# Kernel optimization log

Measured on AMD Instinct MI355X. Metric: run time of the kernel, lower is better.

Reference implementation:

```python
import jax, jax.numpy as jnp
import numpy as np

N_AGENTS = 8192
OBS_DIM = 520
EMBED = 64
HID = 128
N_ACT = 6


def setup_inputs() -> dict:
    key = jax.random.key(0)
    ks = jax.random.split(key, 16)
    s = 0.05  # small init scale for numerical stability
    return {
        "obs": jax.random.normal(ks[0], (N_AGENTS, OBS_DIM), jnp.float32),
        "beliefs": jax.random.normal(ks[1], (N_AGENTS, HID), jnp.float32),
        "W1": jax.random.normal(ks[2], (OBS_DIM, EMBED), jnp.float32) * s,
        "b1": jnp.zeros((EMBED,), jnp.float32),
        "W2": jax.random.normal(ks[3], (EMBED, EMBED), jnp.float32) * s,
        "b2": jnp.zeros((EMBED,), jnp.float32),
        "Wb": jax.random.normal(ks[4], (HID, EMBED), jnp.float32) * s,
        "bb": jnp.zeros((EMBED,), jnp.float32),
        "Wg": jax.random.normal(ks[5], (2 * EMBED, HID), jnp.float32) * s,
        "bg": jnp.zeros((HID,), jnp.float32),
        "Wir": jax.random.normal(ks[6], (HID, HID), jnp.float32) * s,
        "Wiz": jax.random.normal(ks[7], (HID, HID), jnp.float32) * s,
        "Win": jax.random.normal(ks[8], (HID, HID), jnp.float32) * s,
        "Whr": jax.random.normal(ks[9], (HID, HID), jnp.float32) * s,
        "bhr": jnp.zeros((HID,), jnp.float32),
        "Whz": jax.random.normal(ks[10], (HID, HID), jnp.float32) * s,
        "bhz": jnp.zeros((HID,), jnp.float32),
        "Whn": jax.random.normal(ks[11], (HID, HID), jnp.float32) * s,
        "bhn": jnp.zeros((HID,), jnp.float32),
        "Wout": jax.random.normal(ks[12], (HID, N_ACT), jnp.float32) * s,
        "bout": jnp.zeros((N_ACT,), jnp.float32),
    }


def reference(obs, beliefs, W1, b1, W2, b2, Wb, bb, Wg, bg,
              Wir, Wiz, Win, Whr, bhr, Whz, bhz, Whn, bhn, Wout, bout):
    n_agents = obs.shape[0]
    # obs MLP: Dense -> relu -> Dense -> relu  [A, EMBED]
    h_obs = jax.nn.relu(obs @ W1 + b1)
    h_obs = jax.nn.relu(h_obs @ W2 + b2)
    # belief projection [A, EMBED]
    bp = beliefs @ Wb + bb
    # self-attention over beliefs with diagonal masked out
    attn_logits = (bp @ bp.T) / jnp.sqrt(jnp.asarray(EMBED, bp.dtype))
    attn_logits = attn_logits + jnp.eye(n_agents, dtype=bp.dtype) * (-1e8)
    attn_weights = jax.nn.softmax(attn_logits, axis=-1)
    contexts = attn_weights @ bp  # [A, EMBED]
    # GRU input projection [A, HID]
    gru_in = jnp.concatenate([h_obs, contexts], axis=-1) @ Wg + bg
    # flax GRUCell (input denses bias-free, hidden denses biased)
    r = jax.nn.sigmoid(gru_in @ Wir + beliefs @ Whr + bhr)
    z = jax.nn.sigmoid(gru_in @ Wiz + beliefs @ Whz + bhz)
    n = jnp.tanh(gru_in @ Win + r * (beliefs @ Whn + bhn))
    new_beliefs = (1.0 - z) * n + z * beliefs
    logits = new_beliefs @ Wout + bout
    return (logits, new_beliefs)
```

## Files before the change

### kernel.cpp

```cpp
#include <hip/hip_runtime.h>

#define A_N 8192
#define OBS_D 520
#define EMB 64
#define HID 128
#define NACT 6
#define SPLIT 16

typedef short bf16x8 __attribute__((ext_vector_type(8)));
typedef _Float16 half8 __attribute__((ext_vector_type(8)));
typedef float f32x4 __attribute__((ext_vector_type(4)));
typedef unsigned short u16;
typedef unsigned int u32;

#define MFMA_BF(a,b,c) __builtin_amdgcn_mfma_f32_16x16x32_bf16(a,b,c,0,0,0)
#define MFMA_FH(a,b,c) __builtin_amdgcn_mfma_f32_16x16x32_f16(a,b,c,0,0,0)

__device__ inline u32 fbits(float f){ union{float f; u32 u;}v; v.f=f; return v.u; }
__device__ inline float fval(u32 u){ union{u32 u; float f;}v; v.u=u; return v.f; }
__device__ inline u16 f2bf(float f){ u32 u=fbits(f); u += 0x7fffu + ((u>>16)&1u); return (u16)(u>>16); }
__device__ inline u32 pk_bf(float pe, float po){
  return __builtin_amdgcn_perm(fbits(po), fbits(pe), 0x07060302u);
}
__device__ inline float sigmoidf_fast(float x){
  x = fminf(fmaxf(x, -30.f), 30.f);
  return 1.f / (1.f + __expf(-x));
}
__device__ inline float tanhf_fast(float x){
  x = fminf(fmaxf(x, -15.f), 15.f);
  float e = __expf(-2.f*x);
  return (1.f - e) / (1.f + e);
}

#define EXP2C 0.18033688011112042f

__global__ __launch_bounds__(256) void kPrep2(
    const float* __restrict__ Wg, const float* __restrict__ Wir,
    const float* __restrict__ Wiz, const float* __restrict__ Win,
    const float* __restrict__ Whr, const float* __restrict__ Whz,
    const float* __restrict__ Whn, const float* __restrict__ W1,
    const float* __restrict__ W2, const float* __restrict__ Wb,
    const float* __restrict__ beliefs, const float* __restrict__ bb,
    _Float16* __restrict__ WT, _Float16* __restrict__ W1T,
    _Float16* __restrict__ W2T, u16* __restrict__ bp, u16* __restrict__ bpT)
{
  __shared__ float tile[64][65];
  __shared__ u16 WbL[64][136];
  const int t = threadIdx.x, b = blockIdx.x;

  if (b < 38) {
    const float* src; int k0, c0, srcStride, kValid;
    if (b < 28) {
      const int mi = b >> 2, tl = b & 3;
      src = mi==0?Wg: mi==1?Wir: mi==2?Wiz: mi==3?Win: mi==4?Whr: mi==5?Whz: Whn;
      k0 = (tl >> 1) * 64; c0 = (tl & 1) * 64; srcStride = 128; kValid = 128;
    } else if (b < 37) {
      src = W1; k0 = (b - 28) * 64; c0 = 0; srcStride = 64; kValid = OBS_D;
    } else {
      src = W2; k0 = 0; c0 = 0; srcStride = 64; kValid = 64;
    }
    #pragma unroll
    for (int i = 0; i < 16; i++) {
      const int idx = i * 256 + t;
      const int rr = idx >> 6, cc = idx & 63;
      tile[rr][cc] = (k0 + rr < kValid) ? src[(size_t)(k0 + rr) * srcStride + c0 + cc] : 0.f;
    }
    __syncthreads();
    if (b < 28) {
      const int mi = b >> 2;
      _Float16* dst = WT + (size_t)mi * 16384;
      #pragma unroll
      for (int i = 0; i < 16; i++) {
        const int idx = i * 256 + t;
        const int rr = idx >> 6, cc = idx & 63;
        dst[(size_t)(c0 + rr) * 128 + k0 + cc] = (_Float16)tile[cc][rr];
      }
    } else if (b < 37) {
      #pragma unroll
      for (int i = 0; i < 16; i++) {
        const int idx = i * 256 + t;
        const int rr = idx >> 6, cc = idx & 63;
        if (k0 + cc < 544)
          W1T[(size_t)rr * 544 + k0 + cc] = (_Float16)tile[cc][rr];
      }
    } else {
      #pragma unroll
      for (int i = 0; i < 16; i++) {
        const int idx = i * 256 + t;
        const int rr = idx >> 6, cc = idx & 63;
        W2T[(size_t)rr * 64 + cc] = (_Float16)tile[cc][rr];
      }
    }
  } else {
    const int lane = t & 63, wid = t >> 6;
    const int m = lane & 15, quad = lane >> 4;
    const int r0 = (b - 38) * 64 + wid * 16;

    #pragma unroll
    for (int i = 0; i < 8; i++) {
      const int i4 = i * 256 + t;
      float4 w4 = ((const float4*)Wb)[i4];
      const int k = i4 >> 4, c = (i4 & 15) * 4;
      WbL[c+0][k] = f2bf(w4.x); WbL[c+1][k] = f2bf(w4.y);
      WbL[c+2][k] = f2bf(w4.z); WbL[c+3][k] = f2bf(w4.w);
    }
    __syncthreads();

    f32x4 acc[4];
    #pragma unroll
    for (int ct = 0; ct < 4; ct++) acc[ct] = (f32x4){0.f,0.f,0.f,0.f};
    #pragma unroll
    for (int s = 0; s < 4; s++) {
      const int k0 = s*32;
      const float* ap = beliefs + (size_t)(r0+m)*HID + k0 + quad*8;
      float4 a0 = *(const float4*)ap;
      float4 a1 = *(const float4*)(ap + 4);
      union { u16 e[8]; bf16x8 v; } av;
      av.e[0]=f2bf(a0.x); av.e[1]=f2bf(a0.y); av.e[2]=f2bf(a0.z); av.e[3]=f2bf(a0.w);
      av.e[4]=f2bf(a1.x); av.e[5]=f2bf(a1.y); av.e[6]=f2bf(a1.z); av.e[7]=f2bf(a1.w);
      #pragma unroll
      for (int ct = 0; ct < 4; ct++) {
        bf16x8 bw = *(const bf16x8*)&WbL[ct*16+m][k0 + quad*8];
        acc[ct] = MFMA_BF(av.v, bw, acc[ct]);
      }
    }
    #pragma unroll
    for (int ct = 0; ct < 4; ct++) {
      const int col = ct*16 + m;
      const float bbv = bb[col];
      u16 e[4];
      #pragma unroll
      for (int r = 0; r < 4; r++) e[r] = f2bf(acc[ct][r] + bbv);
      #pragma unroll
      for (int r = 0; r < 4; r++)
        bp[(size_t)(r0 + quad*4 + r)*EMB + col] = e[r];
      uint2 pkv;
      pkv.x = (u32)e[0] | ((u32)e[1] << 16);
      pkv.y = (u32)e[2] | ((u32)e[3] << 16);
      *(uint2*)(bpT + (size_t)col*A_N + r0 + quad*4) = pkv;
    }
  }
}

__global__ __launch_bounds__(256) void kM(
    const u16* __restrict__ bp, const u16* __restrict__ bpT,
    u16* __restrict__ ctxp, float* __restrict__ sums,
    const float* __restrict__ obs, const _Float16* __restrict__ W1T,
    const float* __restrict__ b1, const _Float16* __restrict__ W2T,
    const float* __restrict__ b2, _Float16* __restrict__ h2f)
{
  __shared__ __align__(16) u16 P[4][4][16 * 72];
  const int lane = threadIdx.x & 63;
  const int wid  = threadIdx.x >> 6;
  const int m = lane & 15, quad = lane >> 4;

  if (blockIdx.x < 512) {
    const int w = blockIdx.x * 4 + wid;
    const int split = w >> 7;
    const int qt = w & 127;
    const int q0 = qt * 64;

    bf16x8 qa[4][2];
    #pragma unroll
    for (int f = 0; f < 4; f++) {
      const u16* qr = bp + (size_t)(q0 + f*16 + m)*EMB + quad*8;
      qa[f][0] = *(const bf16x8*)(qr);
      qa[f][1] = *(const bf16x8*)(qr + 32);
    }
    f32x4 oacc[4][4];
    #pragma unroll
    for (int f = 0; f < 4; f++)
      #pragma unroll
      for (int d = 0; d < 4; d++) oacc[f][d] = (f32x4){0.f,0.f,0.f,0.f};
    float rowsum[4] = {0.f, 0.f, 0.f, 0.f};

    const int kbeg = split * (A_N / SPLIT);
    const int kend = kbeg + (A_N / SPLIT);

    for (int k0 = kbeg; k0 < kend; k0 += 64) {
      #pragma unroll
      for (int jt = 0; jt < 4; jt++) {
        const u16* kr = bp + (size_t)(k0 + jt*16 + m)*EMB + quad*8;
        const bf16x8 kb0 = *(const bf16x8*)(kr);
        const bf16x8 kb1 = *(const bf16x8*)(kr + 32);
        #pragma unroll
        for (int f = 0; f < 4; f++) {
          f32x4 s = (f32x4){0.f,0.f,0.f,0.f};
          s = MFMA_BF(kb0, qa[f][0], s);
          s = MFMA_BF(kb1, qa[f][1], s);
          float p0 = __builtin_amdgcn_exp2f(s[0]*EXP2C);
          float p1 = __builtin_amdgcn_exp2f(s[1]*EXP2C);
          float p2 = __builtin_amdgcn_exp2f(s[2]*EXP2C);
          float p3 = __builtin_amdgcn_exp2f(s[3]*EXP2C);
          if ((k0 + jt*16) == (q0 + f*16)) {
            const int jl = quad*4;
            if (jl + 0 == m) p0 = 0.f;
            if (jl + 1 == m) p1 = 0.f;
            if (jl + 2 == m) p2 = 0.f;
            if (jl + 3 == m) p3 = 0.f;
          }
          rowsum[f] += (p0 + p1) + (p2 + p3);
          uint2 pkv; pkv.x = pk_bf(p0, p1); pkv.y = pk_bf(p2, p3);
          *(uint2*)&P[wid][f][m*72 + jt*16 + quad*4] = pkv;
        }
      }
      bf16x8 vb[4][2];
      #pragma unroll
      for (int dtt = 0; dtt < 4; dtt++) {
        const u16* vr = bpT + (size_t)(dtt*16+m)*A_N + k0 + quad*8;
        vb[dtt][0] = *(const bf16x8*)(vr);
        vb[dtt][1] = *(const bf16x8*)(vr + 32);
      }
      asm volatile("s_waitcnt lgkmcnt(0)" ::: "memory");
      #pragma unroll
      for (int f = 0; f < 4; f++) {
        const bf16x8 pa0 = *(const bf16x8*)&P[wid][f][m*72 + quad*8];
        const bf16x8 pa1 = *(const bf16x8*)&P[wid][f][m*72 + 32 + quad*8];
        #pragma unroll
        for (int dtt = 0; dtt < 4; dtt++) {
          oacc[f][dtt] = MFMA_BF(pa0, vb[dtt][0], oacc[f][dtt]);
          oacc[f][dtt] = MFMA_BF(pa1, vb[dtt][1], oacc[f][dtt]);
        }
      }
    }

    #pragma unroll
    for (int f = 0; f < 4; f++) {
      float v = rowsum[f];
      v += __shfl_xor(v, 16, 64);
      v += __shfl_xor(v, 32, 64);
      if (lane < 16)
        sums[(size_t)split*A_N + q0 + f*16 + lane] = v;
    }
    #pragma unroll
    for (int f = 0; f < 4; f++) {
      const size_t base = ((size_t)split*A_N + q0 + f*16) * EMB;
      #pragma unroll
      for (int dtt = 0; dtt < 4; dtt++)
        #pragma unroll
        for (int r = 0; r < 4; r++)
          ctxp[base + (size_t)(quad*4+r)*EMB + dtt*16 + m] = f2bf(oacc[f][dtt][r]);
    }
  } else {
    const int r0 = (blockIdx.x - 512) * 64 + wid * 16;
    f32x4 oa[4];
    #pragma unroll
    for (int ct = 0; ct < 4; ct++) oa[ct] = (f32x4){0.f,0.f,0.f,0.f};

    for (int s = 0; s < 17; s++) {
      const int k0 = s * 32;
      union { _Float16 e[8]; half8 v; } af;
      if (s < 16) {
        const float* ap = obs + (size_t)(r0+m)*OBS_D + k0 + quad*8;
        float4 a0 = *(const float4*)ap;
        float4 a1 = *(const float4*)(ap + 4);
        af.e[0]=(_Float16)a0.x; af.e[1]=(_Float16)a0.y; af.e[2]=(_Float16)a0.z; af.e[3]=(_Float16)a0.w;
        af.e[4]=(_Float16)a1.x; af.e[5]=(_Float16)a1.y; af.e[6]=(_Float16)a1.z; af.e[7]=(_Float16)a1.w;
      } else {
        #pragma unroll
        for (int j = 0; j < 8; j++) af.e[j] = (_Float16)0.f;
        if (quad == 0) {
          const float* ap = obs + (size_t)(r0+m)*OBS_D + 512;
          float4 a0 = *(const float4*)ap;
          float4 a1 = *(const float4*)(ap + 4);
          af.e[0]=(_Float16)a0.x; af.e[1]=(_Float16)a0.y; af.e[2]=(_Float16)a0.z; af.e[3]=(_Float16)a0.w;
          af.e[4]=(_Float16)a1.x; af.e[5]=(_Float16)a1.y; af.e[6]=(_Float16)a1.z; af.e[7]=(_Float16)a1.w;
        }
      }
      #pragma unroll
      for (int ct = 0; ct < 4; ct++) {
        half8 bw = *(const half8*)(W1T + (size_t)(ct*16+m)*544 + k0 + quad*8);
        oa[ct] = MFMA_FH(af.v, bw, oa[ct]);
      }
    }
    _Float16* H1 = (_Float16*)&P[wid][0][0];
    #pragma unroll
    for (int ct = 0; ct < 4; ct++) {
      const float b1v = b1[ct*16 + m];
      #pragma unroll
      for (int r = 0; r < 4; r++) {
        float v = fmaxf(oa[ct][r] + b1v, 0.f);
        H1[(quad*4+r)*72 + ct*16 + m] = (_Float16)v;
      }
    }
    __syncthreads();
    f32x4 ob[4];
    #pragma unroll
    for (int ct = 0; ct < 4; ct++) ob[ct] = (f32x4){0.f,0.f,0.f,0.f};
    #pragma unroll
    for (int s2 = 0; s2 < 2; s2++) {
      half8 ah = *(const half8*)(H1 + m*72 + s2*32 + quad*8);
      #pragma unroll
      for (int ct = 0; ct < 4; ct++) {
        half8 bw = *(const half8*)(W2T + (size_t)(ct*16+m)*64 + s2*32 + quad*8);
        ob[ct] = MFMA_FH(ah, bw, ob[ct]);
      }
    }
    #pragma unroll
    for (int ct = 0; ct < 4; ct++) {
      const float b2v = b2[ct*16 + m];
      #pragma unroll
      for (int r = 0; r < 4; r++) {
        float v = fmaxf(ob[ct][r] + b2v, 0.f);
        h2f[(size_t)(r0 + quad*4 + r)*EMB + ct*16 + m] = (_Float16)v;
      }
    }
  }
}

__global__ __launch_bounds__(256) void kRed(
    const u16* __restrict__ ctxp, const float* __restrict__ sums,
    _Float16* __restrict__ xh)
{
  const int idx = blockIdx.x * 256 + threadIdx.x;
  const int row = idx >> 5;
  const int cp  = idx & 31;
  float s0 = 0.f, s1 = 0.f, ss = 0.f;
  #pragma unroll
  for (int sp = 0; sp < SPLIT; sp++) {
    const u32 u = *(const u32*)(ctxp + ((size_t)sp*A_N + row)*EMB + cp*2);
    s0 += fval(u << 16);
    s1 += fval(u & 0xffff0000u);
    ss += sums[(size_t)sp*A_N + row];
  }
  const float inv = 1.f / ss;
  union { _Float16 e[2]; u32 u; } o;
  o.e[0] = (_Float16)(s0 * inv);
  o.e[1] = (_Float16)(s1 * inv);
  *(u32*)(xh + (size_t)row*EMB + cp*2) = o.u;
}

__global__ __launch_bounds__(256) void k3_gru(
    const float* __restrict__ beliefs, const _Float16* __restrict__ h2f,
    const _Float16* __restrict__ xh,
    const _Float16* __restrict__ WT,
    const float* __restrict__ bg, const float* __restrict__ bhr,
    const float* __restrict__ bhz, const float* __restrict__ bhn,
    const float* __restrict__ Wout, const float* __restrict__ bout,
    float* __restrict__ out)
{
  __shared__ _Float16 xf[32][136];
  __shared__ _Float16 belf[32][136];
  __shared__ _Float16 gruf[32][136];
  const int t = threadIdx.x;
  const int lane = t & 63, wid = t >> 6;
  const int m = lane & 15, quad = lane >> 4;
  const int r0 = blockIdx.x * 32;

  #pragma unroll
  for (int i = 0; i < 2; i++) {
    const int idx = i*256 + t;
    const int row = idx >> 4, seg = idx & 15;
    const float* bpR = beliefs + (size_t)(r0+row)*HID + seg*8;
    float4 a0 = *(const float4*)bpR;
    float4 a1 = *(const float4*)(bpR + 4);
    union { _Float16 e[8]; half8 v; } hb;
    hb.e[0]=(_Float16)a0.x; hb.e[1]=(_Float16)a0.y; hb.e[2]=(_Float16)a0.z; hb.e[3]=(_Float16)a0.w;
    hb.e[4]=(_Float16)a1.x; hb.e[5]=(_Float16)a1.y; hb.e[6]=(_Float16)a1.z; hb.e[7]=(_Float16)a1.w;
    *(half8*)&belf[row][seg*8] = hb.v;
  }
  #pragma unroll
  for (int i = 0; i < 2; i++) {
    const int idx = i*256 + t;
    const int row = idx >> 4, seg = idx & 15;
    if (seg < 8) {
      half8 hv = *(const half8*)(h2f + (size_t)(r0+row)*EMB + seg*8);
      *(half8*)&xf[row][seg*8] = hv;
    } else {
      half8 xv = *(const half8*)(xh + (size_t)(r0+row)*EMB + (seg-8)*8);
      *(half8*)&xf[row][64 + (seg-8)*8] = xv;
    }
  }
  __syncthreads();

  f32x4 g[2][2];
  #pragma unroll
  for (int rt = 0; rt < 2; rt++)
    #pragma unroll
    for (int ci = 0; ci < 2; ci++) g[rt][ci] = (f32x4){0.f,0.f,0.f,0.f};
  #pragma unroll
  for (int s = 0; s < 4; s++) {
    half8 bw0 = *(const half8*)(WT + (size_t)((wid*2+0)*16+m)*128 + s*32 + quad*8);
    half8 bw1 = *(const half8*)(WT + (size_t)((wid*2+1)*16+m)*128 + s*32 + quad*8);
    #pragma unroll
    for (int rt = 0; rt < 2; rt++) {
      half8 ax = *(const half8*)&xf[rt*16 + m][s*32 + quad*8];
      g[rt][0] = MFMA_FH(ax, bw0, g[rt][0]);
      g[rt][1] = MFMA_FH(ax, bw1, g[rt][1]);
    }
  }
  #pragma unroll
  for (int rt = 0; rt < 2; rt++)
    #pragma unroll
    for (int ci = 0; ci < 2; ci++) {
      const int col = (wid*2+ci)*16 + m;
      const float bgv = bg[col];
      #pragma unroll
      for (int r = 0; r < 4; r++)
        gruf[rt*16 + quad*4 + r][col] = (_Float16)(g[rt][ci][r] + bgv);
    }
  __syncthreads();

  f32x4 RV[2][2], ZV[2][2];
  #pragma unroll
  for (int gidx = 0; gidx < 3; gidx++) {
    const _Float16* WiTg = WT + (size_t)(1+gidx)*16384;
    const _Float16* WhTg = WT + (size_t)(4+gidx)*16384;
    f32x4 gi[2][2], gh[2][2];
    #pragma unroll
    for (int rt = 0; rt < 2; rt++)
      #pragma unroll
      for (int ci = 0; ci < 2; ci++) {
        gi[rt][ci] = (f32x4){0.f,0.f,0.f,0.f};
        gh[rt][ci] = (f32x4){0.f,0.f,0.f,0.f};
      }
    #pragma unroll
    for (int s = 0; s < 4; s++) {
      half8 bi0 = *(const half8*)(WiTg + (size_t)((wid*2+0)*16+m)*128 + s*32 + quad*8);
      half8 bi1 = *(const half8*)(WiTg + (size_t)((wid*2+1)*16+m)*128 + s*32 + quad*8);
      half8 bh0 = *(const half8*)(WhTg + (size_t)((wid*2+0)*16+m)*128 + s*32 + quad*8);
      half8 bh1 = *(const half8*)(WhTg + (size_t)((wid*2+1)*16+m)*128 + s*32 + quad*8);
      #pragma unroll
      for (int rt = 0; rt < 2; rt++) {
        half8 ag = *(const half8*)&gruf[rt*16 + m][s*32 + quad*8];
        half8 ab = *(const half8*)&belf[rt*16 + m][s*32 + quad*8];
        gi[rt][0] = MFMA_FH(ag, bi0, gi[rt][0]);
        gi[rt][1] = MFMA_FH(ag, bi1, gi[rt][1]);
        gh[rt][0] = MFMA_FH(ab, bh0, gh[rt][0]);
        gh[rt][1] = MFMA_FH(ab, bh1, gh[rt][1]);
      }
    }
    if (gidx == 0) {
      #pragma unroll
      for (int rt = 0; rt < 2; rt++)
        #pragma unroll
        for (int ci = 0; ci < 2; ci++) {
          const float bv = bhr[(wid*2+ci)*16 + m];
          #pragma unroll
          for (int r = 0; r < 4; r++)
            RV[rt][ci][r] = sigmoidf_fast(gi[rt][ci][r] + gh[rt][ci][r] + bv);
        }
    } else if (gidx == 1) {
      #pragma unroll
      for (int rt = 0; rt < 2; rt++)
        #pragma unroll
        for (int ci = 0; ci < 2; ci++) {
          const float bv = bhz[(wid*2+ci)*16 + m];
          #pragma unroll
          for (int r = 0; r < 4; r++)
            ZV[rt][ci][r] = sigmoidf_fast(gi[rt][ci][r] + gh[rt][ci][r] + bv);
        }
    } else {
      #pragma unroll
      for (int rt = 0; rt < 2; rt++)
        #pragma unroll
        for (int ci = 0; ci < 2; ci++) {
          const int col = (wid*2+ci)*16 + m;
          const float bv = bhn[col];
          #pragma unroll
          for (int r = 0; r < 4; r++) {
            const int row = rt*16 + quad*4 + r;
            float bel = beliefs[(size_t)(r0+row)*HID + col];
            float pre = gi[rt][ci][r] + RV[rt][ci][r] * (gh[rt][ci][r] + bv);
            float nv = tanhf_fast(pre);
            float nb = (1.f - ZV[rt][ci][r]) * nv + ZV[rt][ci][r] * bel;
            out[(size_t)NACT*A_N + (size_t)(r0+row)*HID + col] = nb;
            xf[row][col] = (_Float16)nb;
          }
        }
    }
  }
  __syncthreads();

  if (t < 32*NACT) {
    const int row = t / NACT, c = t % NACT;
    float a = bout[c];
    #pragma unroll 8
    for (int k = 0; k < HID; k++)
      a += (float)xf[row][k] * Wout[(size_t)k*NACT + c];
    out[(size_t)(r0+row)*NACT + c] = a;
  }
}

extern "C" void kernel_launch(void* const* d_in, const int* in_sizes, int n_in,
                              void* d_out, int out_size, void* d_ws, size_t ws_size,
                              hipStream_t stream) {
  const float* obs     = (const float*)d_in[0];
  const float* beliefs = (const float*)d_in[1];
  const float* W1      = (const float*)d_in[2];
  const float* b1      = (const float*)d_in[3];
  const float* W2      = (const float*)d_in[4];
  const float* b2      = (const float*)d_in[5];
  const float* Wb      = (const float*)d_in[6];
  const float* bb      = (const float*)d_in[7];
  const float* Wg      = (const float*)d_in[8];
  const float* bg      = (const float*)d_in[9];
  const float* Wir     = (const float*)d_in[10];
  const float* Wiz     = (const float*)d_in[11];
  const float* Win     = (const float*)d_in[12];
  const float* Whr     = (const float*)d_in[13];
  const float* bhr     = (const float*)d_in[14];
  const float* Whz     = (const float*)d_in[15];
  const float* bhz     = (const float*)d_in[16];
  const float* Whn     = (const float*)d_in[17];
  const float* bhn     = (const float*)d_in[18];
  const float* Wout    = (const float*)d_in[19];
  const float* bout    = (const float*)d_in[20];
  float* out = (float*)d_out;

  char* ws = (char*)d_ws;
  _Float16* h2f  = (_Float16*)(ws);
  u16*      bp   = (u16*)(ws + 1048576);
  u16*      bpT  = (u16*)(ws + 2097152);
  u16*      ctxp = (u16*)(ws + 3145728);
  float*    sums = (float*)(ws + 19922944);
  _Float16* WT   = (_Float16*)(ws + 20447232);
  _Float16* W1T  = (_Float16*)(ws + 20676608);
  _Float16* W2T  = (_Float16*)(ws + 20746240);
  _Float16* xh   = (_Float16*)(ws + 1048576);

  hipLaunchKernelGGL(kPrep2, dim3(166), dim3(256), 0, stream,
                     Wg, Wir, Wiz, Win, Whr, Whz, Whn, W1, W2, Wb, beliefs, bb,
                     WT, W1T, W2T, bp, bpT);
  hipLaunchKernelGGL(kM, dim3(640), dim3(256), 0, stream,
                     bp, bpT, ctxp, sums, obs, W1T, b1, W2T, b2, h2f);
  hipLaunchKernelGGL(kRed, dim3(1024), dim3(256), 0, stream, ctxp, sums, xh);
  hipLaunchKernelGGL(k3_gru, dim3(256), dim3(256), 0, stream,
                     beliefs, h2f, xh, WT, bg, bhr, bhz, bhn, Wout, bout, out);
}
```

Before: 176.9 us.

## Fuse split-context reduction into GRU kernel and coalesce new-belief stores

Removes the separate kRed launch and folds the split-K reduction of attention partial contexts and softmax sums into the GRU kernel's prologue, with each thread reading 16-byte chunks. Reorders kM so the obs-MLP blocks occupy the low block indices. The GRU epilogue now takes beliefs from the fp16 shared copy instead of reloading fp32 from global memory. New beliefs are written as coalesced float4 rows after a barrier, and Wout is staged in shared memory. This saves one launch and an intermediate round trip, at the cost of fp16 rounding of beliefs in the blend and new beliefs stored from their fp16-rounded values.

```diff
diff --git a/kernel.cpp b/kernel.cpp
--- a/kernel.cpp
+++ b/kernel.cpp
@@ -154,8 +154,8 @@
   const int wid  = threadIdx.x >> 6;
   const int m = lane & 15, quad = lane >> 4;
 
-  if (blockIdx.x < 512) {
-    const int w = blockIdx.x * 4 + wid;
+  if (blockIdx.x >= 128) {
+    const int w = (blockIdx.x - 128) * 4 + wid;
     const int split = w >> 7;
     const int qt = w & 127;
     const int q0 = qt * 64;
@@ -242,7 +242,7 @@
           ctxp[base + (size_t)(quad*4+r)*EMB + dtt*16 + m] = f2bf(oacc[f][dtt][r]);
     }
   } else {
-    const int r0 = (blockIdx.x - 512) * 64 + wid * 16;
+    const int r0 = blockIdx.x * 64 + wid * 16;
     f32x4 oa[4];
     #pragma unroll
     for (int ct = 0; ct < 4; ct++) oa[ct] = (f32x4){0.f,0.f,0.f,0.f};
@@ -308,40 +308,19 @@
   }
 }
 
-__global__ __launch_bounds__(256) void kRed(
-    const u16* __restrict__ ctxp, const float* __restrict__ sums,
-    _Float16* __restrict__ xh)
-{
-  const int idx = blockIdx.x * 256 + threadIdx.x;
-  const int row = idx >> 5;
-  const int cp  = idx & 31;
-  float s0 = 0.f, s1 = 0.f, ss = 0.f;
-  #pragma unroll
-  for (int sp = 0; sp < SPLIT; sp++) {
-    const u32 u = *(const u32*)(ctxp + ((size_t)sp*A_N + row)*EMB + cp*2);
-    s0 += fval(u << 16);
-    s1 += fval(u & 0xffff0000u);
-    ss += sums[(size_t)sp*A_N + row];
-  }
-  const float inv = 1.f / ss;
-  union { _Float16 e[2]; u32 u; } o;
-  o.e[0] = (_Float16)(s0 * inv);
-  o.e[1] = (_Float16)(s1 * inv);
-  *(u32*)(xh + (size_t)row*EMB + cp*2) = o.u;
-}
-
 __global__ __launch_bounds__(256) void k3_gru(
     const float* __restrict__ beliefs, const _Float16* __restrict__ h2f,
-    const _Float16* __restrict__ xh,
+    const u16* __restrict__ ctxp, const float* __restrict__ sums,
     const _Float16* __restrict__ WT,
     const float* __restrict__ bg, const float* __restrict__ bhr,
     const float* __restrict__ bhz, const float* __restrict__ bhn,
     const float* __restrict__ Wout, const float* __restrict__ bout,
     float* __restrict__ out)
 {
-  __shared__ _Float16 xf[32][136];
-  __shared__ _Float16 belf[32][136];
-  __shared__ _Float16 gruf[32][136];
+  __shared__ __align__(16) _Float16 xf[32][136];
+  __shared__ __align__(16) _Float16 belf[32][136];
+  __shared__ __align__(16) _Float16 gruf[32][136];
+  __shared__ float invs[32];
   const int t = threadIdx.x;
   const int lane = t & 63, wid = t >> 6;
   const int m = lane & 15, quad = lane >> 4;
@@ -359,17 +338,35 @@
     hb.e[4]=(_Float16)a1.x; hb.e[5]=(_Float16)a1.y; hb.e[6]=(_Float16)a1.z; hb.e[7]=(_Float16)a1.w;
     *(half8*)&belf[row][seg*8] = hb.v;
   }
-  #pragma unroll
-  for (int i = 0; i < 2; i++) {
-    const int idx = i*256 + t;
-    const int row = idx >> 4, seg = idx & 15;
-    if (seg < 8) {
-      half8 hv = *(const half8*)(h2f + (size_t)(r0+row)*EMB + seg*8);
-      *(half8*)&xf[row][seg*8] = hv;
-    } else {
-      half8 xv = *(const half8*)(xh + (size_t)(r0+row)*EMB + (seg-8)*8);
-      *(half8*)&xf[row][64 + (seg-8)*8] = xv;
-    }
+  const int crow = t >> 3, cg = t & 7;
+  {
+    half8 hv = *(const half8*)(h2f + (size_t)(r0+crow)*EMB + cg*8);
+    *(half8*)&xf[crow][cg*8] = hv;
+  }
+  float ca[8];
+  #pragma unroll
+  for (int d = 0; d < 8; d++) ca[d] = 0.f;
+  #pragma unroll
+  for (int sp = 0; sp < SPLIT; sp++) {
+    uint4 u = *(const uint4*)(ctxp + ((size_t)sp*A_N + r0 + crow)*EMB + cg*8);
+    ca[0] += fval(u.x << 16); ca[1] += fval(u.x & 0xffff0000u);
+    ca[2] += fval(u.y << 16); ca[3] += fval(u.y & 0xffff0000u);
+    ca[4] += fval(u.z << 16); ca[5] += fval(u.z & 0xffff0000u);
+    ca[6] += fval(u.w << 16); ca[7] += fval(u.w & 0xffff0000u);
+  }
+  if (t < 32) {
+    float ss = 0.f;
+    #pragma unroll
+    for (int sp = 0; sp < SPLIT; sp++) ss += sums[(size_t)sp*A_N + r0 + t];
+    invs[t] = 1.f / ss;
+  }
+  __syncthreads();
+  {
+    const float iv = invs[crow];
+    union { _Float16 e[8]; half8 v; } hc;
+    #pragma unroll
+    for (int d = 0; d < 8; d++) hc.e[d] = (_Float16)(ca[d] * iv);
+    *(half8*)&xf[crow][64 + cg*8] = hc.v;
   }
   __syncthreads();
 
@@ -460,15 +457,27 @@
           #pragma unroll
           for (int r = 0; r < 4; r++) {
             const int row = rt*16 + quad*4 + r;
-            float bel = beliefs[(size_t)(r0+row)*HID + col];
+            float bel = (float)belf[row][col];
             float pre = gi[rt][ci][r] + RV[rt][ci][r] * (gh[rt][ci][r] + bv);
             float nv = tanhf_fast(pre);
             float nb = (1.f - ZV[rt][ci][r]) * nv + ZV[rt][ci][r] * bel;
-            out[(size_t)NACT*A_N + (size_t)(r0+row)*HID + col] = nb;
             xf[row][col] = (_Float16)nb;
           }
         }
     }
+  }
+  __syncthreads();
+
+  float* woutL = (float*)&gruf[0][0];
+  if (t < 192) ((float4*)woutL)[t] = ((const float4*)Wout)[t];
+  #pragma unroll
+  for (int i = 0; i < 4; i++) {
+    const int lin = i*256 + t;
+    const int row = lin >> 5, c4 = (lin & 31) * 4;
+    float4 o;
+    o.x = (float)xf[row][c4+0]; o.y = (float)xf[row][c4+1];
+    o.z = (float)xf[row][c4+2]; o.w = (float)xf[row][c4+3];
+    *(float4*)&out[(size_t)NACT*A_N + (size_t)(r0+row)*HID + c4] = o;
   }
   __syncthreads();
 
@@ -477,7 +486,7 @@
     float a = bout[c];
     #pragma unroll 8
     for (int k = 0; k < HID; k++)
-      a += (float)xf[row][k] * Wout[(size_t)k*NACT + c];
+      a += (float)xf[row][k] * woutL[k*NACT + c];
     out[(size_t)(r0+row)*NACT + c] = a;
   }
 }
@@ -517,14 +526,12 @@
   _Float16* WT   = (_Float16*)(ws + 20447232);
   _Float16* W1T  = (_Float16*)(ws + 20676608);
   _Float16* W2T  = (_Float16*)(ws + 20746240);
-  _Float16* xh   = (_Float16*)(ws + 1048576);
 
   hipLaunchKernelGGL(kPrep2, dim3(166), dim3(256), 0, stream,
                      Wg, Wir, Wiz, Win, Whr, Whz, Whn, W1, W2, Wb, beliefs, bb,
                      WT, W1T, W2T, bp, bpT);
   hipLaunchKernelGGL(kM, dim3(640), dim3(256), 0, stream,
                      bp, bpT, ctxp, sums, obs, W1T, b1, W2T, b2, h2f);
-  hipLaunchKernelGGL(kRed, dim3(1024), dim3(256), 0, stream, ctxp, sums, xh);
   hipLaunchKernelGGL(k3_gru, dim3(256), dim3(256), 0, stream,
-                     beliefs, h2f, xh, WT, bg, bhr, bhz, bhn, Wout, bout, out);
-}
+                     beliefs, h2f, ctxp, sums, WT, bg, bhr, bhz, bhn, Wout, bout, out);
+}
```

After: 167.4 us. 1.06x faster.
